# Kernel tuning notes

Measured on AMD Instinct MI355X. Metric: run time of the kernel, lower is better.

## Reference

```python
import jax, jax.numpy as jnp
import numpy as np

N, E, G = 50000, 640000, 16384
F_IN, H = 128, 128
EPS = 1e-5
_BN_S = 1.0 / np.sqrt(1.0 + EPS)  # BatchNorm1d eval mode: running_mean=0, running_var=1


def _forward(floats, edge_src, edge_dst, game_indices):
    (x, in_bn_g, in_bn_b, lin_W, lin_b, bn0_g, bn0_b,
     cW1, cb1, bn1_g, bn1_b, cW2, cb2, bn2_g, bn2_b, cW3, cb3, bn3_g, bn3_b,
     hW1, hb1, hbn_g, hbn_b, hW2, hb2, hW3, hb3,
     oW1, ob1, obn1_g, obn1_b, oW2, ob2, obn2_g, obn2_b, oW3, ob3) = floats
    n = x.shape[0]

    def bn(z, g, b):  # eval-mode BN with zero running mean, unit running var
        return g * (z * _BN_S) + b

    # GCN symmetric normalization with self-loops: deg_i = 1 + in_degree_i
    deg = jnp.ones((n,), x.dtype).at[edge_dst].add(1.0)
    dis = jax.lax.rsqrt(deg)
    coef = (dis[edge_src] * dis[edge_dst])[:, None]      # [E,1]
    self_coef = (dis * dis)[:, None]                      # [N,1] self-loop weight 1/deg

    def gcn(h, W, b):
        hw = h @ W                                        # [N,H]
        agg = jax.ops.segment_sum(hw[edge_src] * coef, edge_dst, num_segments=n)
        return agg + hw * self_coef + b

    h = bn(x, in_bn_g, in_bn_b)
    h = jax.nn.relu(bn(h @ lin_W + lin_b, bn0_g, bn0_b))
    h = h + jax.nn.relu(bn(gcn(h, cW1, cb1), bn1_g, bn1_b))
    h = h + jax.nn.relu(bn(gcn(h, cW2, cb2), bn2_g, bn2_b))
    h = h + jax.nn.relu(bn(gcn(h, cW3, cb3), bn3_g, bn3_b))

    xg = h[game_indices]                                  # [G,H]
    z = jnp.einsum('gf,hfo->hgo', xg, hW1) + hb1[:, None, :]
    z = jax.nn.relu(hbn_g[:, None, :] * (z * _BN_S) + hbn_b[:, None, :])
    z = jax.nn.relu(jnp.einsum('hgo,hok->hgk', z, hW2) + hb2[:, None, :])
    heads = (jnp.einsum('hgk,hko->hgo', z, hW3) + hb3[:, None, :])[:, :, 0].T  # [G,4]
    # outcome classification head -> [G,3]
    o = jax.nn.relu(bn(xg @ oW1 + ob1, obn1_g, obn1_b))
    o = jax.nn.relu(bn(o @ oW2 + ob2, obn2_g, obn2_b))
    o = o @ oW3 + ob3
    # columns: home_goals, away_goals, home_shots, away_shots, outcome_logits(3)
    return jnp.concatenate([heads, o], axis=-1)          # [G,7]


def setup_inputs() -> dict:
    key = jax.random.key(0)
    ks = iter(jax.random.split(key, 64))
    f32 = jnp.float32

    def rn(shape, s=0.05):
        return jax.random.normal(next(ks), shape, f32) * s

    H2, H4 = H // 2, H // 4
    return {
        'x': jax.random.normal(next(ks), (N, F_IN), f32),
        'edge_src': jax.random.randint(next(ks), (E,), 0, N),
        'edge_dst': jax.random.randint(next(ks), (E,), 0, N),
        'game_indices': jax.random.randint(next(ks), (G,), 0, N),
        'in_bn_g': jnp.ones((F_IN,), f32), 'in_bn_b': jnp.zeros((F_IN,), f32),
        'lin_W': rn((F_IN, H)), 'lin_b': jnp.zeros((H,), f32),
        'bn0_g': jnp.ones((H,), f32), 'bn0_b': jnp.zeros((H,), f32),
        'cW1': rn((H, H)), 'cb1': jnp.zeros((H,), f32),
        'bn1_g': jnp.ones((H,), f32), 'bn1_b': jnp.zeros((H,), f32),
        'cW2': rn((H, H)), 'cb2': jnp.zeros((H,), f32),
        'bn2_g': jnp.ones((H,), f32), 'bn2_b': jnp.zeros((H,), f32),
        'cW3': rn((H, H)), 'cb3': jnp.zeros((H,), f32),
        'bn3_g': jnp.ones((H,), f32), 'bn3_b': jnp.zeros((H,), f32),
        'hW1': rn((4, H, H2)), 'hb1': jnp.zeros((4, H2), f32),
        'hbn_g': jnp.ones((4, H2), f32), 'hbn_b': jnp.zeros((4, H2), f32),
        'hW2': rn((4, H2, H4)), 'hb2': jnp.zeros((4, H4), f32),
        'hW3': rn((4, H4, 1)), 'hb3': jnp.zeros((4, 1), f32),
        'oW1': rn((H, H2)), 'ob1': jnp.zeros((H2,), f32),
        'obn1_g': jnp.ones((H2,), f32), 'obn1_b': jnp.zeros((H2,), f32),
        'oW2': rn((H2, H4)), 'ob2': jnp.zeros((H4,), f32),
        'obn2_g': jnp.ones((H4,), f32), 'obn2_b': jnp.zeros((H4,), f32),
        'oW3': rn((H4, 3)), 'ob3': jnp.zeros((3,), f32),
    }


def reference(x, edge_src, edge_dst, game_indices, in_bn_g, in_bn_b, lin_W, lin_b,
              bn0_g, bn0_b, cW1, cb1, bn1_g, bn1_b, cW2, cb2, bn2_g, bn2_b,
              cW3, cb3, bn3_g, bn3_b, hW1, hb1, hbn_g, hbn_b, hW2, hb2, hW3, hb3,
              oW1, ob1, obn1_g, obn1_b, oW2, ob2, obn2_g, obn2_b, oW3, ob3):
    floats = (x, in_bn_g, in_bn_b, lin_W, lin_b, bn0_g, bn0_b,
              cW1, cb1, bn1_g, bn1_b, cW2, cb2, bn2_g, bn2_b, cW3, cb3, bn3_g, bn3_b,
              hW1, hb1, hbn_g, hbn_b, hW2, hb2, hW3, hb3,
              oW1, ob1, obn1_g, obn1_b, oW2, ob2, obn2_g, obn2_b, oW3, ob3)
    return _forward(floats, edge_src, edge_dst, game_indices)
```

## Files before the change

kernel.cpp:

```cpp
#include <hip/hip_runtime.h>
#include <hip/hip_bf16.h>

#define HDIM 128
#define PAD 64
static constexpr float BN_S = 0.99999500003749968751f;

typedef float f32x4 __attribute__((ext_vector_type(4)));
typedef short s16x8 __attribute__((ext_vector_type(8)));

union U128 { uint4 u; s16x8 s; };

__device__ __forceinline__ unsigned short f2bs(float f){
    union{float f; unsigned u;} c; c.f = f;
    unsigned r = c.u + 0x7fffu + ((c.u >> 16) & 1u);
    return (unsigned short)(r >> 16);
}
__device__ __forceinline__ float bs2f(unsigned short s){
    union{unsigned u; float f;} c; c.u = ((unsigned)s) << 16;
    return c.f;
}
__device__ __forceinline__ float ulo(unsigned u){ union{unsigned i; float f;} c; c.i = u << 16; return c.f; }
__device__ __forceinline__ float uhi(unsigned u){ union{unsigned i; float f;} c; c.i = u & 0xffff0000u; return c.f; }

__global__ __launch_bounds__(256) void k_prepcount(
    const float* __restrict__ linW, const float* __restrict__ cW1,
    const float* __restrict__ cW2, const float* __restrict__ cW3,
    const float* __restrict__ hW1, const float* __restrict__ oW1,
    const float* __restrict__ hW2, const float* __restrict__ oW2,
    unsigned short* __restrict__ wf, unsigned short* __restrict__ p1,
    unsigned short* __restrict__ p2,
    const int* __restrict__ esrc, const int* __restrict__ edst,
    int* __restrict__ cnt, int* __restrict__ slots, int E)
{
    int id = blockIdx.x * 256 + threadIdx.x;
    if (id < 65536){
        int mat = id >> 14;
        int el = id & 16383;
        int k = el >> 7, n = el & 127;
        const float* W = (mat == 0) ? linW : (mat == 1) ? cW1 : (mat == 2) ? cW2 : cW3;
        float v = W[k * 128 + n];
        unsigned short hs = f2bs(v);
        unsigned short ls = f2bs(v - bs2f(hs));
        int nt = n >> 4, lanen = n & 15, kc = k >> 5, quad = (k >> 3) & 3, j = k & 7;
        int lane = quad * 16 + lanen;
        size_t base = (size_t)mat * 32768;
        wf[base + (size_t)(((nt * 4 + kc) * 2 + 0) * 64 + lane) * 8 + j] = hs;
        wf[base + (size_t)(((nt * 4 + kc) * 2 + 1) * 64 + lane) * 8 + j] = ls;
    } else if (id < 65536 + 51200){
        int id1 = id - 65536;
        if (id1 < 40960){
            int j = id1 & 7, lane = (id1 >> 3) & 63, kc = (id1 >> 9) & 3, nt = (id1 >> 11) & 3, y = id1 >> 13;
            int k = kc * 32 + (lane >> 4) * 8 + j;
            int n = nt * 16 + (lane & 15);
            float w = (y < 4) ? hW1[(y * 128 + k) * 64 + n] : oW1[k * 64 + n];
            p1[id1] = f2bs(w);
        } else {
            int id2 = id1 - 40960;
            int j = id2 & 7, lane = (id2 >> 3) & 63, kc = (id2 >> 9) & 1, nt = (id2 >> 10) & 1, y = id2 >> 11;
            int k = kc * 32 + (lane >> 4) * 8 + j;
            int n = nt * 16 + (lane & 15);
            float w = (y < 4) ? hW2[(y * 64 + k) * 32 + n] : oW2[k * 32 + n];
            p2[id2] = f2bs(w);
        }
    } else {
        int e = id - (65536 + 51200);
        if (e < E){
            int d = edst[e];
            int r = atomicAdd(&cnt[d], 1);
            if (r < PAD) slots[(size_t)d * PAD + r] = esrc[e];
        }
    }
}

__device__ __forceinline__ void gemm01_tile(
    int tile, const float* __restrict__ A,
    const uint4* __restrict__ wf0, const uint4* __restrict__ wf1,
    const float* __restrict__ ing, const float* __restrict__ inb,
    const float* __restrict__ ebias, const float* __restrict__ eg, const float* __restrict__ eb,
    const int* __restrict__ cnt,
    float* __restrict__ hout, unsigned short* __restrict__ hwout, int nrows,
    unsigned* sbuf, float* sdis)
{
    unsigned* sAhi = sbuf;
    unsigned* sAlo = sbuf + 64 * 68;
    int t = threadIdx.x;
    int row0 = tile * 64;
    if (t < 64){
        int gr = row0 + t;
        sdis[t] = (gr < nrows) ? rsqrtf(1.0f + (float)cnt[gr]) : 1.0f;
    }
    for (int i = t; i < 2048; i += 256){
        int r = i >> 5, q = i & 31;
        int gr = row0 + r;
        float4 v = make_float4(0.f, 0.f, 0.f, 0.f);
        if (gr < nrows) v = *(const float4*)&A[(size_t)gr * 128 + q * 4];
        float4 g = *(const float4*)&ing[q * 4];
        float4 bo = *(const float4*)&inb[q * 4];
        v.x = v.x * (g.x * BN_S) + bo.x;
        v.y = v.y * (g.y * BN_S) + bo.y;
        v.z = v.z * (g.z * BN_S) + bo.z;
        v.w = v.w * (g.w * BN_S) + bo.w;
        unsigned u0 = __float_as_uint(v.x), u1 = __float_as_uint(v.y);
        unsigned u2 = __float_as_uint(v.z), u3 = __float_as_uint(v.w);
        uint2 hi = make_uint2((u0 >> 16) | (u1 & 0xffff0000u), (u2 >> 16) | (u3 & 0xffff0000u));
        unsigned short l0 = f2bs(v.x - __uint_as_float(u0 & 0xffff0000u));
        unsigned short l1 = f2bs(v.y - __uint_as_float(u1 & 0xffff0000u));
        unsigned short l2 = f2bs(v.z - __uint_as_float(u2 & 0xffff0000u));
        unsigned short l3 = f2bs(v.w - __uint_as_float(u3 & 0xffff0000u));
        uint2 lo = make_uint2((unsigned)l0 | ((unsigned)l1 << 16), (unsigned)l2 | ((unsigned)l3 << 16));
        *(uint2*)&sAhi[r * 68 + q * 2] = hi;
        *(uint2*)&sAlo[r * 68 + q * 2] = lo;
    }
    __syncthreads();

    int w = t >> 6, l = t & 63;
    int lanen = l & 15, quad = l >> 4;
    int mrow = w * 16 + lanen;
    f32x4 acc[8];
#pragma unroll
    for (int i = 0; i < 8; ++i) acc[i] = (f32x4){0.f, 0.f, 0.f, 0.f};

#pragma unroll 1
    for (int kc = 0; kc < 4; ++kc){
        U128 ahi, alo;
        ahi.u = *(const uint4*)&sAhi[mrow * 68 + kc * 16 + quad * 4];
        alo.u = *(const uint4*)&sAlo[mrow * 68 + kc * 16 + quad * 4];
        U128 whi[8];
#pragma unroll
        for (int nt = 0; nt < 8; ++nt)
            whi[nt].u = wf0[((nt * 4 + kc) * 2 + 0) * 64 + l];
#pragma unroll
        for (int nt = 0; nt < 8; ++nt)
            acc[nt] = __builtin_amdgcn_mfma_f32_16x16x32_bf16(ahi.s, whi[nt].s, acc[nt], 0, 0, 0);
#pragma unroll
        for (int nt = 0; nt < 8; ++nt)
            acc[nt] = __builtin_amdgcn_mfma_f32_16x16x32_bf16(alo.s, whi[nt].s, acc[nt], 0, 0, 0);
    }

    __syncthreads();
    float* so = (float*)sbuf;
#pragma unroll
    for (int nt = 0; nt < 8; ++nt){
        int n = nt * 16 + lanen;
        float bias = ebias[n], g = eg[n], bo = eb[n];
#pragma unroll
        for (int r = 0; r < 4; ++r){
            int row = w * 16 + quad * 4 + r;
            float v = g * ((acc[nt][r] + bias) * BN_S) + bo;
            so[row * 132 + n] = fmaxf(v, 0.f);
        }
    }
    __syncthreads();
    for (int i = t; i < 2048; i += 256){
        int row = i >> 5, c4 = (i & 31) * 4;
        int grow = row0 + row;
        if (grow < nrows)
            *(float4*)&hout[(size_t)grow * 128 + c4] = *(float4*)&so[row * 132 + c4];
    }

    f32x4 acc2[8];
#pragma unroll
    for (int i = 0; i < 8; ++i) acc2[i] = (f32x4){0.f, 0.f, 0.f, 0.f};
#pragma unroll 1
    for (int kc = 0; kc < 4; ++kc){
        float4 a0 = *(const float4*)&so[mrow * 132 + kc * 32 + quad * 8];
        float4 a1 = *(const float4*)&so[mrow * 132 + kc * 32 + quad * 8 + 4];
        U128 af;
        af.u.x = (unsigned)f2bs(a0.x) | ((unsigned)f2bs(a0.y) << 16);
        af.u.y = (unsigned)f2bs(a0.z) | ((unsigned)f2bs(a0.w) << 16);
        af.u.z = (unsigned)f2bs(a1.x) | ((unsigned)f2bs(a1.y) << 16);
        af.u.w = (unsigned)f2bs(a1.z) | ((unsigned)f2bs(a1.w) << 16);
        U128 wh[8];
#pragma unroll
        for (int nt = 0; nt < 8; ++nt)
            wh[nt].u = wf1[((nt * 4 + kc) * 2 + 0) * 64 + l];
#pragma unroll
        for (int nt = 0; nt < 8; ++nt)
            acc2[nt] = __builtin_amdgcn_mfma_f32_16x16x32_bf16(af.s, wh[nt].s, acc2[nt], 0, 0, 0);
    }
    __syncthreads();
    unsigned short* ss = (unsigned short*)sbuf;
#pragma unroll
    for (int nt = 0; nt < 8; ++nt){
        int n = nt * 16 + lanen;
#pragma unroll
        for (int r = 0; r < 4; ++r){
            int row = w * 16 + quad * 4 + r;
            ss[row * 136 + n] = f2bs(acc2[nt][r] * sdis[row]);
        }
    }
    __syncthreads();
    for (int i = t; i < 1024; i += 256){
        int row = i >> 4, c = i & 15;
        int grow = row0 + row;
        if (grow < nrows)
            *(uint4*)&hwout[(size_t)grow * 128 + c * 8] = *(uint4*)&ss[row * 136 + c * 8];
    }
}

__global__ __launch_bounds__(256) void k_cg01(
    const float* __restrict__ x, const uint4* __restrict__ wf0, const uint4* __restrict__ wf1,
    const float* __restrict__ ing, const float* __restrict__ inb,
    const float* __restrict__ lb, const float* __restrict__ g0, const float* __restrict__ b0,
    const int* __restrict__ cnt,
    float* __restrict__ hbuf, unsigned short* __restrict__ hwb, int nrows)
{
    __shared__ __align__(16) unsigned sbuf[64 * 136];
    __shared__ float sdis[64];
    gemm01_tile(blockIdx.x, x, wf0, wf1, ing, inb, lb, g0, b0, cnt, hbuf, hwb, nrows, sbuf, sdis);
}

__global__ __launch_bounds__(256) void k_gemmb(
    const uint4* __restrict__ hb16, const uint4* __restrict__ wf,
    const int* __restrict__ cnt,
    unsigned short* __restrict__ hwout, int nrows)
{
    __shared__ __align__(16) unsigned sbuf[64 * 68];
    __shared__ float sdis[64];
    int t = threadIdx.x;
    int row0 = blockIdx.x * 64;
    if (t < 64){
        int gr = row0 + t;
        sdis[t] = (gr < nrows) ? rsqrtf(1.0f + (float)cnt[gr]) : 1.0f;
    }
    for (int i = t; i < 1024; i += 256){
        int r = i >> 4, c = i & 15;
        int gr = row0 + r;
        uint4 v = make_uint4(0u, 0u, 0u, 0u);
        if (gr < nrows) v = hb16[(size_t)gr * 16 + c];
        *(uint4*)&sbuf[r * 68 + c * 4] = v;
    }
    __syncthreads();

    int w = t >> 6, l = t & 63;
    int lanen = l & 15, quad = l >> 4;
    int mrow = w * 16 + lanen;
    f32x4 acc[8];
#pragma unroll
    for (int i = 0; i < 8; ++i) acc[i] = (f32x4){0.f, 0.f, 0.f, 0.f};
#pragma unroll 1
    for (int kc = 0; kc < 4; ++kc){
        U128 ah;
        ah.u = *(const uint4*)&sbuf[mrow * 68 + kc * 16 + quad * 4];
        U128 wh[8];
#pragma unroll
        for (int nt = 0; nt < 8; ++nt)
            wh[nt].u = wf[((nt * 4 + kc) * 2 + 0) * 64 + l];
#pragma unroll
        for (int nt = 0; nt < 8; ++nt)
            acc[nt] = __builtin_amdgcn_mfma_f32_16x16x32_bf16(ah.s, wh[nt].s, acc[nt], 0, 0, 0);
    }
    __syncthreads();
    unsigned short* ss = (unsigned short*)sbuf;
#pragma unroll
    for (int nt = 0; nt < 8; ++nt){
        int n = nt * 16 + lanen;
#pragma unroll
        for (int r = 0; r < 4; ++r){
            int row = w * 16 + quad * 4 + r;
            ss[row * 136 + n] = f2bs(acc[nt][r] * sdis[row]);
        }
    }
    __syncthreads();
    for (int i = t; i < 1024; i += 256){
        int row = i >> 4, c = i & 15;
        int grow = row0 + row;
        if (grow < nrows)
            *(uint4*)&hwout[(size_t)grow * 128 + c * 8] = *(uint4*)&ss[row * 136 + c * 8];
    }
}

template<int WRITEH>
__device__ __forceinline__ void agg_body(
    const unsigned* __restrict__ hwu, float* __restrict__ h,
    const int* __restrict__ cnt, const int* __restrict__ slots,
    const float* __restrict__ cb, const float* __restrict__ bg, const float* __restrict__ bb,
    uint4* __restrict__ hb16o, int N)
{
    int row = blockIdx.x * 4 + (threadIdx.x >> 6);
    if (row >= N) return;
    int l = threadIdx.x & 63;
    int sub = l >> 4, cg = l & 15;
    int c0 = cnt[row];
    int c = (c0 > PAD) ? PAD : c0;
    float acc[8];
#pragma unroll
    for (int i = 0; i < 8; ++i) acc[i] = 0.f;
    for (int p = 0; p < c; p += 16){
        int base = p + sub * 4;
        if (base < c){
            int4 s4 = *(const int4*)&slots[(size_t)row * PAD + base];
            int i1 = (base + 1 < c) ? s4.y : s4.x;
            int i2 = (base + 2 < c) ? s4.z : s4.x;
            int i3 = (base + 3 < c) ? s4.w : s4.x;
            float m1 = (base + 1 < c) ? 1.f : 0.f;
            float m2 = (base + 2 < c) ? 1.f : 0.f;
            float m3 = (base + 3 < c) ? 1.f : 0.f;
            uint4 v0 = *(const uint4*)&hwu[(size_t)s4.x * 64 + cg * 4];
            uint4 v1 = *(const uint4*)&hwu[(size_t)i1 * 64 + cg * 4];
            uint4 v2 = *(const uint4*)&hwu[(size_t)i2 * 64 + cg * 4];
            uint4 v3 = *(const uint4*)&hwu[(size_t)i3 * 64 + cg * 4];
            acc[0] += ulo(v0.x); acc[1] += uhi(v0.x);
            acc[2] += ulo(v0.y); acc[3] += uhi(v0.y);
            acc[4] += ulo(v0.z); acc[5] += uhi(v0.z);
            acc[6] += ulo(v0.w); acc[7] += uhi(v0.w);
            acc[0] = fmaf(ulo(v1.x), m1, acc[0]); acc[1] = fmaf(uhi(v1.x), m1, acc[1]);
            acc[2] = fmaf(ulo(v1.y), m1, acc[2]); acc[3] = fmaf(uhi(v1.y), m1, acc[3]);
            acc[4] = fmaf(ulo(v1.z), m1, acc[4]); acc[5] = fmaf(uhi(v1.z), m1, acc[5]);
            acc[6] = fmaf(ulo(v1.w), m1, acc[6]); acc[7] = fmaf(uhi(v1.w), m1, acc[7]);
            acc[0] = fmaf(ulo(v2.x), m2, acc[0]); acc[1] = fmaf(uhi(v2.x), m2, acc[1]);
            acc[2] = fmaf(ulo(v2.y), m2, acc[2]); acc[3] = fmaf(uhi(v2.y), m2, acc[3]);
            acc[4] = fmaf(ulo(v2.z), m2, acc[4]); acc[5] = fmaf(uhi(v2.z), m2, acc[5]);
            acc[6] = fmaf(ulo(v2.w), m2, acc[6]); acc[7] = fmaf(uhi(v2.w), m2, acc[7]);
            acc[0] = fmaf(ulo(v3.x), m3, acc[0]); acc[1] = fmaf(uhi(v3.x), m3, acc[1]);
            acc[2] = fmaf(ulo(v3.y), m3, acc[2]); acc[3] = fmaf(uhi(v3.y), m3, acc[3]);
            acc[4] = fmaf(ulo(v3.z), m3, acc[4]); acc[5] = fmaf(uhi(v3.z), m3, acc[5]);
            acc[6] = fmaf(ulo(v3.w), m3, acc[6]); acc[7] = fmaf(uhi(v3.w), m3, acc[7]);
        }
    }
#pragma unroll
    for (int i = 0; i < 8; ++i){
        acc[i] += __shfl_xor(acc[i], 16);
        acc[i] += __shfl_xor(acc[i], 32);
    }
    if (sub == 0){
        float d = rsqrtf(1.0f + (float)c0);
        uint4 sv = *(const uint4*)&hwu[(size_t)row * 64 + cg * 4];
        float sf[8] = {ulo(sv.x), uhi(sv.x), ulo(sv.y), uhi(sv.y),
                       ulo(sv.z), uhi(sv.z), ulo(sv.w), uhi(sv.w)};
        float4 c0v = *(const float4*)&cb[cg * 8], c1v = *(const float4*)&cb[cg * 8 + 4];
        float4 g0v = *(const float4*)&bg[cg * 8], g1v = *(const float4*)&bg[cg * 8 + 4];
        float4 b0v = *(const float4*)&bb[cg * 8], b1v = *(const float4*)&bb[cg * 8 + 4];
        float cc[8] = {c0v.x, c0v.y, c0v.z, c0v.w, c1v.x, c1v.y, c1v.z, c1v.w};
        float gg[8] = {g0v.x, g0v.y, g0v.z, g0v.w, g1v.x, g1v.y, g1v.z, g1v.w};
        float bo[8] = {b0v.x, b0v.y, b0v.z, b0v.w, b1v.x, b1v.y, b1v.z, b1v.w};
        float4 cur0 = *(const float4*)&h[(size_t)row * 128 + cg * 8];
        float4 cur1 = *(const float4*)&h[(size_t)row * 128 + cg * 8 + 4];
        float o[8] = {cur0.x, cur0.y, cur0.z, cur0.w, cur1.x, cur1.y, cur1.z, cur1.w};
#pragma unroll
        for (int i = 0; i < 8; ++i){
            float v = gg[i] * (((acc[i] + sf[i]) * d + cc[i]) * BN_S) + bo[i];
            o[i] += fmaxf(v, 0.f);
        }
        if (WRITEH){
            *(float4*)&h[(size_t)row * 128 + cg * 8] = make_float4(o[0], o[1], o[2], o[3]);
            *(float4*)&h[(size_t)row * 128 + cg * 8 + 4] = make_float4(o[4], o[5], o[6], o[7]);
        }
        uint4 pk;
        pk.x = (unsigned)f2bs(o[0]) | ((unsigned)f2bs(o[1]) << 16);
        pk.y = (unsigned)f2bs(o[2]) | ((unsigned)f2bs(o[3]) << 16);
        pk.z = (unsigned)f2bs(o[4]) | ((unsigned)f2bs(o[5]) << 16);
        pk.w = (unsigned)f2bs(o[6]) | ((unsigned)f2bs(o[7]) << 16);
        hb16o[(size_t)row * 16 + cg] = pk;
    }
}

__global__ __launch_bounds__(256) void k_agg(
    const unsigned* __restrict__ hwu, float* __restrict__ h,
    const int* __restrict__ cnt, const int* __restrict__ slots,
    const float* __restrict__ cb, const float* __restrict__ bg, const float* __restrict__ bb,
    uint4* __restrict__ hb16o, int N)
{
    agg_body<1>(hwu, h, cnt, slots, cb, bg, bb, hb16o, N);
}

__global__ __launch_bounds__(256) void k_agg3(
    const unsigned* __restrict__ hwu, float* __restrict__ h,
    const int* __restrict__ cnt, const int* __restrict__ slots,
    const float* __restrict__ cb, const float* __restrict__ bg, const float* __restrict__ bb,
    uint4* __restrict__ hb16o, int N)
{
    agg_body<0>(hwu, h, cnt, slots, cb, bg, bb, hb16o, N);
}

__global__ __launch_bounds__(256) void k_headmm(
    const uint4* __restrict__ hb16, const int* __restrict__ gidx,
    const uint4* __restrict__ p1v, const uint4* __restrict__ p2v,
    const float* __restrict__ hb1, const float* __restrict__ hg1, const float* __restrict__ hbb1,
    const float* __restrict__ hb2,
    const float* __restrict__ hW3, const float* __restrict__ hb3,
    const float* __restrict__ ob1, const float* __restrict__ og1, const float* __restrict__ obb1,
    const float* __restrict__ ob2, const float* __restrict__ og2, const float* __restrict__ obb2,
    const float* __restrict__ oW3, const float* __restrict__ ob3,
    float* __restrict__ out, int G)
{
    __shared__ __align__(16) unsigned sxg[64 * 68];
    __shared__ __align__(16) unsigned sz1u[64 * 36];
    __shared__ __align__(16) unsigned sz2u[64 * 20];
    __shared__ float sb1[64], sg1[64], sbb1[64];
    __shared__ float sb2[32], sg2[32], sbb2[32];
    __shared__ float sW3[96];
    __shared__ float sb3[3];
    __shared__ int sgi[64];

    int t = threadIdx.x;
    int gblk = blockIdx.x;
    int y = blockIdx.y;
    bool bn2 = (y == 4);
    int w = t >> 6, l = t & 63;
    int lanen = l & 15, quad = l >> 4;

    const float* b1  = bn2 ? ob1  : (hb1 + y * 64);
    const float* g1  = bn2 ? og1  : (hg1 + y * 64);
    const float* bb1 = bn2 ? obb1 : (hbb1 + y * 64);
    const float* b2  = bn2 ? ob2  : (hb2 + y * 32);
    const float* W3  = bn2 ? oW3  : (hW3 + y * 32);
    const float* b3  = bn2 ? ob3  : (hb3 + y);
    int nc3 = bn2 ? 3 : 1;

    if (t < 64){
        sb1[t] = b1[t]; sg1[t] = g1[t]; sbb1[t] = bb1[t];
        if (t < 3) sb3[t] = (t < nc3) ? b3[t] : 0.f;
    } else if (t < 96){
        int p = t - 64;
        sb2[p] = b2[p];
        sg2[p] = bn2 ? og2[p] : 1.f;
        sbb2[p] = bn2 ? obb2[p] : 0.f;
    } else if (t < 192){
        int i = t - 96;
        sW3[i] = (i < 32 * nc3) ? W3[i] : 0.f;
    } else {
        int r = t - 192;
        int g = gblk * 64 + r;
        sgi[r] = (g < G) ? gidx[g] : 0;
    }
    __syncthreads();
    for (int i = t; i < 1024; i += 256){
        int r = i >> 4, c = i & 15;
        int node = sgi[r];
        uint4 v = hb16[(size_t)node * 16 + c];
        *(uint4*)&sxg[r * 68 + c * 4] = v;
    }
    __syncthreads();

    f32x4 acc1[4] = {{0.f,0.f,0.f,0.f},{0.f,0.f,0.f,0.f},{0.f,0.f,0.f,0.f},{0.f,0.f,0.f,0.f}};
#pragma unroll
    for (int kc = 0; kc < 4; ++kc){
        U128 a;
        a.u = *(const uint4*)&sxg[(w * 16 + lanen) * 68 + kc * 16 + quad * 4];
#pragma unroll
        for (int nt = 0; nt < 4; ++nt){
            U128 bfr;
            bfr.u = p1v[((y * 4 + nt) * 4 + kc) * 64 + l];
            acc1[nt] = __builtin_amdgcn_mfma_f32_16x16x32_bf16(a.s, bfr.s, acc1[nt], 0, 0, 0);
        }
    }
    {
        unsigned short* sz1s = (unsigned short*)sz1u;
#pragma unroll
        for (int nt = 0; nt < 4; ++nt){
            int n = nt * 16 + lanen;
            float g = sg1[n], bia = sb1[n], bt = sbb1[n];
#pragma unroll
            for (int r = 0; r < 4; ++r){
                int row = w * 16 + quad * 4 + r;
                float v = g * ((acc1[nt][r] + bia) * BN_S) + bt;
                sz1s[row * 72 + n] = f2bs(fmaxf(v, 0.f));
            }
        }
    }
    __syncthreads();

    f32x4 acc2[2] = {{0.f,0.f,0.f,0.f},{0.f,0.f,0.f,0.f}};
#pragma unroll
    for (int kc = 0; kc < 2; ++kc){
        U128 a;
        a.u = *(const uint4*)&sz1u[(w * 16 + lanen) * 36 + kc * 16 + quad * 4];
#pragma unroll
        for (int nt = 0; nt < 2; ++nt){
            U128 bfr;
            bfr.u = p2v[((y * 2 + nt) * 2 + kc) * 64 + l];
            acc2[nt] = __builtin_amdgcn_mfma_f32_16x16x32_bf16(a.s, bfr.s, acc2[nt], 0, 0, 0);
        }
    }
    {
        unsigned short* sz2s = (unsigned short*)sz2u;
#pragma unroll
        for (int nt = 0; nt < 2; ++nt){
            int n = nt * 16 + lanen;
            float bia = sb2[n], g = sg2[n], bt = sbb2[n];
#pragma unroll
            for (int r = 0; r < 4; ++r){
                int row = w * 16 + quad * 4 + r;
                float v = acc2[nt][r] + bia;
                if (bn2) v = g * (v * BN_S) + bt;
                sz2s[row * 40 + n] = f2bs(fmaxf(v, 0.f));
            }
        }
    }
    __syncthreads();

    const unsigned short* sz2s = (const unsigned short*)sz2u;
    if (!bn2){
        if (t < 64){
            int g = gblk * 64 + t;
            if (g < G){
                float s = sb3[0];
#pragma unroll
                for (int p = 0; p < 32; ++p) s = fmaf(bs2f(sz2s[t * 40 + p]), sW3[p], s);
                out[(size_t)g * 7 + y] = s;
            }
        }
    } else {
        if (t < 192){
            int gl = t / 3, c = t % 3;
            int g = gblk * 64 + gl;
            if (g < G){
                float s = sb3[c];
#pragma unroll
                for (int p = 0; p < 32; ++p) s = fmaf(bs2f(sz2s[gl * 40 + p]), sW3[p * 3 + c], s);
                out[(size_t)g * 7 + 4 + c] = s;
            }
        }
    }
}

extern "C" void kernel_launch(void* const* d_in, const int* in_sizes, int n_in,
                              void* d_out, int out_size, void* d_ws, size_t ws_size,
                              hipStream_t stream)
{
    const float* x    = (const float*)d_in[0];
    const int* esrc   = (const int*)d_in[1];
    const int* edst   = (const int*)d_in[2];
    const int* gidx   = (const int*)d_in[3];
    const float* in_g = (const float*)d_in[4];
    const float* in_b = (const float*)d_in[5];
    const float* lin_W = (const float*)d_in[6];
    const float* lin_b = (const float*)d_in[7];
    const float* bn0_g = (const float*)d_in[8];
    const float* bn0_b = (const float*)d_in[9];
    const float* cW[3] = {(const float*)d_in[10], (const float*)d_in[14], (const float*)d_in[18]};
    const float* cb[3] = {(const float*)d_in[11], (const float*)d_in[15], (const float*)d_in[19]};
    const float* bg[3] = {(const float*)d_in[12], (const float*)d_in[16], (const float*)d_in[20]};
    const float* bb[3] = {(const float*)d_in[13], (const float*)d_in[17], (const float*)d_in[21]};
    const float* hW1 = (const float*)d_in[22];
    const float* hb1 = (const float*)d_in[23];
    const float* hg1 = (const float*)d_in[24];
    const float* hbb1 = (const float*)d_in[25];
    const float* hW2 = (const float*)d_in[26];
    const float* hb2 = (const float*)d_in[27];
    const float* hW3 = (const float*)d_in[28];
    const float* hb3 = (const float*)d_in[29];
    const float* oW1 = (const float*)d_in[30];
    const float* ob1 = (const float*)d_in[31];
    const float* og1 = (const float*)d_in[32];
    const float* obb1 = (const float*)d_in[33];
    const float* oW2 = (const float*)d_in[34];
    const float* ob2 = (const float*)d_in[35];
    const float* og2 = (const float*)d_in[36];
    const float* obb2 = (const float*)d_in[37];
    const float* oW3 = (const float*)d_in[38];
    const float* ob3 = (const float*)d_in[39];

    const int N = in_sizes[0] / HDIM;
    const int E = in_sizes[1];
    const int G = in_sizes[3];

    char* wsp = (char*)d_ws;
    size_t off = 0;
    auto alloc = [&](size_t bytes) -> char* {
        char* p = wsp + off;
        off = (off + bytes + 255) & ~(size_t)255;
        return p;
    };
    int* cnt      = (int*)alloc((size_t)N * 4);
    int* slots    = (int*)alloc((size_t)N * PAD * 4);
    float* hbuf   = (float*)alloc((size_t)N * HDIM * 4);
    unsigned short* hwbA = (unsigned short*)alloc((size_t)N * HDIM * 2);
    unsigned short* hwbB = (unsigned short*)alloc((size_t)N * HDIM * 2);
    unsigned short* hb16 = (unsigned short*)alloc((size_t)N * HDIM * 2);
    unsigned short* p1 = (unsigned short*)alloc(40960 * 2);
    unsigned short* p2 = (unsigned short*)alloc(10240 * 2);
    unsigned short* wf = (unsigned short*)alloc((size_t)4 * 32768 * 2);

    int gb = (N + 63) / 64;
    int prepTot = 65536 + 51200 + E;

    hipMemsetAsync(cnt, 0, (size_t)N * 4, stream);
    k_prepcount<<<dim3((prepTot + 255) / 256), dim3(256), 0, stream>>>(
        lin_W, cW[0], cW[1], cW[2], hW1, oW1, hW2, oW2, wf, p1, p2,
        esrc, edst, cnt, slots, E);
    k_cg01<<<dim3(gb), dim3(256), 0, stream>>>(
        x, (const uint4*)wf, (const uint4*)(wf + (size_t)32768),
        in_g, in_b, lin_b, bn0_g, bn0_b, cnt, hbuf, hwbA, N);
    k_agg<<<dim3((N + 3) / 4), dim3(256), 0, stream>>>(
        (const unsigned*)hwbA, hbuf, cnt, slots, cb[0], bg[0], bb[0], (uint4*)hb16, N);
    k_gemmb<<<dim3(gb), dim3(256), 0, stream>>>(
        (const uint4*)hb16, (const uint4*)(wf + (size_t)2 * 32768), cnt, hwbB, N);
    k_agg<<<dim3((N + 3) / 4), dim3(256), 0, stream>>>(
        (const unsigned*)hwbB, hbuf, cnt, slots, cb[1], bg[1], bb[1], (uint4*)hb16, N);
    k_gemmb<<<dim3(gb), dim3(256), 0, stream>>>(
        (const uint4*)hb16, (const uint4*)(wf + (size_t)3 * 32768), cnt, hwbA, N);
    k_agg3<<<dim3((N + 3) / 4), dim3(256), 0, stream>>>(
        (const unsigned*)hwbA, hbuf, cnt, slots, cb[2], bg[2], bb[2], (uint4*)hb16, N);
    k_headmm<<<dim3((G + 63) / 64, 5), dim3(256), 0, stream>>>(
        (const uint4*)hb16, gidx, (const uint4*)p1, (const uint4*)p2,
        hb1, hg1, hbb1, hb2, hW3, hb3,
        ob1, og1, obb1, ob2, og2, obb2, oW3, ob3,
        (float*)d_out, G);
}
```

Before: 322.2 us.

## Overlap edge bucketing with first GEMM via in-kernel counter; shrink slots to uint16

Edge counting and slot filling move out of the weight-prep kernel into the first GEMM kernel as extra leading blocks. GEMM blocks do their matrix work first, then spin on a global done counter before reading degrees to compute the normalisation. Source indices in the slot table are stored as 16-bit values, which halves slot memory traffic in the three aggregation kernels. The spin-wait relies on all edge blocks being scheduled ahead of or alongside the GEMM blocks, and the 16-bit indices only hold while N is at most 65536.

```diff
diff --git a/kernel.cpp b/kernel.cpp
--- a/kernel.cpp
+++ b/kernel.cpp
@@ -22,15 +22,13 @@
 __device__ __forceinline__ float ulo(unsigned u){ union{unsigned i; float f;} c; c.i = u << 16; return c.f; }
 __device__ __forceinline__ float uhi(unsigned u){ union{unsigned i; float f;} c; c.i = u & 0xffff0000u; return c.f; }
 
-__global__ __launch_bounds__(256) void k_prepcount(
+__global__ __launch_bounds__(256) void k_prep(
     const float* __restrict__ linW, const float* __restrict__ cW1,
     const float* __restrict__ cW2, const float* __restrict__ cW3,
     const float* __restrict__ hW1, const float* __restrict__ oW1,
     const float* __restrict__ hW2, const float* __restrict__ oW2,
     unsigned short* __restrict__ wf, unsigned short* __restrict__ p1,
-    unsigned short* __restrict__ p2,
-    const int* __restrict__ esrc, const int* __restrict__ edst,
-    int* __restrict__ cnt, int* __restrict__ slots, int E)
+    unsigned short* __restrict__ p2)
 {
     int id = blockIdx.x * 256 + threadIdx.x;
     if (id < 65536){
@@ -62,38 +60,46 @@
             float w = (y < 4) ? hW2[(y * 64 + k) * 32 + n] : oW2[k * 32 + n];
             p2[id2] = f2bs(w);
         }
-    } else {
-        int e = id - (65536 + 51200);
+    }
+}
+
+__global__ __launch_bounds__(256) void k_cg01c(
+    const float* __restrict__ x, const uint4* __restrict__ wf0, const uint4* __restrict__ wf1,
+    const float* __restrict__ ing, const float* __restrict__ inb,
+    const float* __restrict__ lb, const float* __restrict__ g0, const float* __restrict__ b0,
+    int* __restrict__ cnt, int* __restrict__ done,
+    float* __restrict__ hout, unsigned short* __restrict__ hwout, int nrows, int nCB,
+    const int* __restrict__ esrc, const int* __restrict__ edst,
+    unsigned short* __restrict__ slots, int E)
+{
+    __shared__ __align__(16) unsigned sbuf[64 * 136];
+    __shared__ float sdis[64];
+    int bid = blockIdx.x;
+    int t = threadIdx.x;
+
+    if (bid < nCB){
+        int e = bid * 256 + t;
         if (e < E){
             int d = edst[e];
             int r = atomicAdd(&cnt[d], 1);
-            if (r < PAD) slots[(size_t)d * PAD + r] = esrc[e];
-        }
-    }
-}
-
-__device__ __forceinline__ void gemm01_tile(
-    int tile, const float* __restrict__ A,
-    const uint4* __restrict__ wf0, const uint4* __restrict__ wf1,
-    const float* __restrict__ ing, const float* __restrict__ inb,
-    const float* __restrict__ ebias, const float* __restrict__ eg, const float* __restrict__ eb,
-    const int* __restrict__ cnt,
-    float* __restrict__ hout, unsigned short* __restrict__ hwout, int nrows,
-    unsigned* sbuf, float* sdis)
-{
+            if (r < PAD) slots[(size_t)d * PAD + r] = (unsigned short)esrc[e];
+        }
+        __threadfence();
+        __syncthreads();
+        if (t == 0)
+            __hip_atomic_fetch_add(done, 1, __ATOMIC_RELEASE, __HIP_MEMORY_SCOPE_AGENT);
+        return;
+    }
+
+    int tile = bid - nCB;
     unsigned* sAhi = sbuf;
     unsigned* sAlo = sbuf + 64 * 68;
-    int t = threadIdx.x;
     int row0 = tile * 64;
-    if (t < 64){
-        int gr = row0 + t;
-        sdis[t] = (gr < nrows) ? rsqrtf(1.0f + (float)cnt[gr]) : 1.0f;
-    }
     for (int i = t; i < 2048; i += 256){
         int r = i >> 5, q = i & 31;
         int gr = row0 + r;
         float4 v = make_float4(0.f, 0.f, 0.f, 0.f);
-        if (gr < nrows) v = *(const float4*)&A[(size_t)gr * 128 + q * 4];
+        if (gr < nrows) v = *(const float4*)&x[(size_t)gr * 128 + q * 4];
         float4 g = *(const float4*)&ing[q * 4];
         float4 bo = *(const float4*)&inb[q * 4];
         v.x = v.x * (g.x * BN_S) + bo.x;
@@ -142,7 +148,7 @@
 #pragma unroll
     for (int nt = 0; nt < 8; ++nt){
         int n = nt * 16 + lanen;
-        float bias = ebias[n], g = eg[n], bo = eb[n];
+        float bias = lb[n], g = g0[n], bo = b0[n];
 #pragma unroll
         for (int r = 0; r < 4; ++r){
             int row = w * 16 + quad * 4 + r;
@@ -178,7 +184,20 @@
         for (int nt = 0; nt < 8; ++nt)
             acc2[nt] = __builtin_amdgcn_mfma_f32_16x16x32_bf16(af.s, wh[nt].s, acc2[nt], 0, 0, 0);
     }
-    __syncthreads();
+
+    if (t == 0){
+        while (__hip_atomic_load(done, __ATOMIC_ACQUIRE, __HIP_MEMORY_SCOPE_AGENT) < nCB)
+            __builtin_amdgcn_s_sleep(2);
+    }
+    __syncthreads();
+    if (t < 64){
+        int gr = row0 + t;
+        int cv = (gr < nrows)
+            ? __hip_atomic_load(&cnt[gr], __ATOMIC_RELAXED, __HIP_MEMORY_SCOPE_AGENT) : 0;
+        sdis[t] = rsqrtf(1.0f + (float)cv);
+    }
+    __syncthreads();
+
     unsigned short* ss = (unsigned short*)sbuf;
 #pragma unroll
     for (int nt = 0; nt < 8; ++nt){
@@ -196,18 +215,6 @@
         if (grow < nrows)
             *(uint4*)&hwout[(size_t)grow * 128 + c * 8] = *(uint4*)&ss[row * 136 + c * 8];
     }
-}
-
-__global__ __launch_bounds__(256) void k_cg01(
-    const float* __restrict__ x, const uint4* __restrict__ wf0, const uint4* __restrict__ wf1,
-    const float* __restrict__ ing, const float* __restrict__ inb,
-    const float* __restrict__ lb, const float* __restrict__ g0, const float* __restrict__ b0,
-    const int* __restrict__ cnt,
-    float* __restrict__ hbuf, unsigned short* __restrict__ hwb, int nrows)
-{
-    __shared__ __align__(16) unsigned sbuf[64 * 136];
-    __shared__ float sdis[64];
-    gemm01_tile(blockIdx.x, x, wf0, wf1, ing, inb, lb, g0, b0, cnt, hbuf, hwb, nrows, sbuf, sdis);
 }
 
 __global__ __launch_bounds__(256) void k_gemmb(
@@ -273,7 +280,7 @@
 template<int WRITEH>
 __device__ __forceinline__ void agg_body(
     const unsigned* __restrict__ hwu, float* __restrict__ h,
-    const int* __restrict__ cnt, const int* __restrict__ slots,
+    const int* __restrict__ cnt, const unsigned short* __restrict__ slots,
     const float* __restrict__ cb, const float* __restrict__ bg, const float* __restrict__ bb,
     uint4* __restrict__ hb16o, int N)
 {
@@ -289,14 +296,18 @@
     for (int p = 0; p < c; p += 16){
         int base = p + sub * 4;
         if (base < c){
-            int4 s4 = *(const int4*)&slots[(size_t)row * PAD + base];
-            int i1 = (base + 1 < c) ? s4.y : s4.x;
-            int i2 = (base + 2 < c) ? s4.z : s4.x;
-            int i3 = (base + 3 < c) ? s4.w : s4.x;
+            uint2 s2 = *(const uint2*)&slots[(size_t)row * PAD + base];
+            int s0 = (int)(s2.x & 0xffffu);
+            int t1 = (int)(s2.x >> 16);
+            int t2 = (int)(s2.y & 0xffffu);
+            int t3 = (int)(s2.y >> 16);
+            int i1 = (base + 1 < c) ? t1 : s0;
+            int i2 = (base + 2 < c) ? t2 : s0;
+            int i3 = (base + 3 < c) ? t3 : s0;
             float m1 = (base + 1 < c) ? 1.f : 0.f;
             float m2 = (base + 2 < c) ? 1.f : 0.f;
             float m3 = (base + 3 < c) ? 1.f : 0.f;
-            uint4 v0 = *(const uint4*)&hwu[(size_t)s4.x * 64 + cg * 4];
+            uint4 v0 = *(const uint4*)&hwu[(size_t)s0 * 64 + cg * 4];
             uint4 v1 = *(const uint4*)&hwu[(size_t)i1 * 64 + cg * 4];
             uint4 v2 = *(const uint4*)&hwu[(size_t)i2 * 64 + cg * 4];
             uint4 v3 = *(const uint4*)&hwu[(size_t)i3 * 64 + cg * 4];
@@ -357,7 +368,7 @@
 
 __global__ __launch_bounds__(256) void k_agg(
     const unsigned* __restrict__ hwu, float* __restrict__ h,
-    const int* __restrict__ cnt, const int* __restrict__ slots,
+    const int* __restrict__ cnt, const unsigned short* __restrict__ slots,
     const float* __restrict__ cb, const float* __restrict__ bg, const float* __restrict__ bb,
     uint4* __restrict__ hb16o, int N)
 {
@@ -366,7 +377,7 @@
 
 __global__ __launch_bounds__(256) void k_agg3(
     const unsigned* __restrict__ hwu, float* __restrict__ h,
-    const int* __restrict__ cnt, const int* __restrict__ slots,
+    const int* __restrict__ cnt, const unsigned short* __restrict__ slots,
     const float* __restrict__ cb, const float* __restrict__ bg, const float* __restrict__ bb,
     uint4* __restrict__ hb16o, int N)
 {
@@ -563,8 +574,9 @@
         off = (off + bytes + 255) & ~(size_t)255;
         return p;
     };
-    int* cnt      = (int*)alloc((size_t)N * 4);
-    int* slots    = (int*)alloc((size_t)N * PAD * 4);
+    int* cnt      = (int*)alloc((size_t)(N + 64) * 4);
+    int* done     = cnt + N;
+    unsigned short* slots = (unsigned short*)alloc((size_t)N * PAD * 2);
     float* hbuf   = (float*)alloc((size_t)N * HDIM * 4);
     unsigned short* hwbA = (unsigned short*)alloc((size_t)N * HDIM * 2);
     unsigned short* hwbB = (unsigned short*)alloc((size_t)N * HDIM * 2);
@@ -574,15 +586,15 @@
     unsigned short* wf = (unsigned short*)alloc((size_t)4 * 32768 * 2);
 
     int gb = (N + 63) / 64;
-    int prepTot = 65536 + 51200 + E;
-
-    hipMemsetAsync(cnt, 0, (size_t)N * 4, stream);
-    k_prepcount<<<dim3((prepTot + 255) / 256), dim3(256), 0, stream>>>(
-        lin_W, cW[0], cW[1], cW[2], hW1, oW1, hW2, oW2, wf, p1, p2,
-        esrc, edst, cnt, slots, E);
-    k_cg01<<<dim3(gb), dim3(256), 0, stream>>>(
+    int nCB = (E + 255) / 256;
+
+    hipMemsetAsync(cnt, 0, (size_t)(N + 64) * 4, stream);
+    k_prep<<<dim3((65536 + 51200 + 255) / 256), dim3(256), 0, stream>>>(
+        lin_W, cW[0], cW[1], cW[2], hW1, oW1, hW2, oW2, wf, p1, p2);
+    k_cg01c<<<dim3(nCB + gb), dim3(256), 0, stream>>>(
         x, (const uint4*)wf, (const uint4*)(wf + (size_t)32768),
-        in_g, in_b, lin_b, bn0_g, bn0_b, cnt, hbuf, hwbA, N);
+        in_g, in_b, lin_b, bn0_g, bn0_b, cnt, done, hbuf, hwbA, N, nCB,
+        esrc, edst, slots, E);
     k_agg<<<dim3((N + 3) / 4), dim3(256), 0, stream>>>(
         (const unsigned*)hwbA, hbuf, cnt, slots, cb[0], bg[0], bb[0], (uint4*)hb16, N);
     k_gemmb<<<dim3(gb), dim3(256), 0, stream>>>(
```

New measurement: 651.8 us. +102.3%, slower.
